# Performance work log

Hardware: AMD Instinct MI355X
Metric: run time of the kernel (lower is better)

## Reference

```python
import jax, jax.numpy as jnp
import numpy as np


def setup_inputs() -> dict:
    key = jax.random.key(0)
    k1, k2 = jax.random.split(key)
    B, S, D = 4, 2048, 1024
    x = jax.random.normal(k1, (B, S, D), dtype=jnp.float32)
    # uniform initializer in keras is small; scale to keep softmax well-behaved
    kernel = jax.random.normal(k2, (3, D, D), dtype=jnp.float32) * 0.02
    return {"x": x, "kernel": kernel}


def reference(x, kernel):
    # x: [B, S, D], kernel: [3, D, D]
    D = x.shape[-1]
    q = jnp.einsum('bsd,de->bse', x, kernel[0])
    k = jnp.einsum('bsd,de->bse', x, kernel[1])
    v = jnp.einsum('bsd,de->bse', x, kernel[2])
    scores = jnp.einsum('bqe,bke->bqk', q, k) / jnp.sqrt(jnp.float32(D))
    attn = jax.nn.softmax(scores, axis=-1)
    return jnp.einsum('bqk,bke->bqe', attn, v)
```

## Files before the change

kernel.cpp:

```cpp
#include <hip/hip_runtime.h>
#include <hip/hip_bf16.h>
#include <cstdint>

typedef __bf16 bf16x8 __attribute__((ext_vector_type(8)));
typedef float f32x4 __attribute__((ext_vector_type(4)));

__device__ __forceinline__ unsigned short f2bf(float f) {
  union { float f; uint32_t u; } a; a.f = f;
  uint32_t r = a.u + 0x7fffu + ((a.u >> 16) & 1u);
  return (unsigned short)(r >> 16);
}
__device__ __forceinline__ void gload_lds16(const unsigned short* g, unsigned short* l) {
  __builtin_amdgcn_global_load_lds(
      (const __attribute__((address_space(1))) void*)g,
      (__attribute__((address_space(3))) void*)l, 16, 0, 0);
}

__global__ void cast_all(const float* __restrict__ x, const float* __restrict__ W,
                         unsigned short* __restrict__ xb, unsigned short* __restrict__ Wt) {
  __shared__ float tile[32][33];
  const int bx = blockIdx.x;
  const int t = threadIdx.x;
  if (bx < 4096) {
    size_t i = ((size_t)bx * 256 + t) * 8;
    float4 a = *(const float4*)(x + i);
    float4 b = *(const float4*)(x + i + 4);
    uint4 o;
    o.x = (uint32_t)f2bf(a.x) | ((uint32_t)f2bf(a.y) << 16);
    o.y = (uint32_t)f2bf(a.z) | ((uint32_t)f2bf(a.w) << 16);
    o.z = (uint32_t)f2bf(b.x) | ((uint32_t)f2bf(b.y) << 16);
    o.w = (uint32_t)f2bf(b.z) | ((uint32_t)f2bf(b.w) << 16);
    *(uint4*)(xb + i) = o;
  } else {
    const int b = bx - 4096;
    const int z = b >> 10;
    const int rest = b & 1023;
    const int bxx = rest & 31, byy = rest >> 5;
    const float* Wz = W + (size_t)z * 1048576;
    unsigned short* Wtz = Wt + (size_t)z * 1048576;
    const int x0 = bxx * 32, y0 = byy * 32;
    const int tx = t & 31, ty = t >> 5;
#pragma unroll
    for (int i = 0; i < 32; i += 8)
      tile[ty + i][tx] = Wz[(size_t)(y0 + ty + i) * 1024 + x0 + tx];
    __syncthreads();
#pragma unroll
    for (int i = 0; i < 32; i += 8)
      Wtz[(size_t)(x0 + ty + i) * 1024 + y0 + tx] = f2bf(tile[tx][ty + i]);
  }
}

template <int MODE>
__global__ void __launch_bounds__(256)
gemm_bt(const unsigned short* __restrict__ Aall,
        const unsigned short* __restrict__ Btall,
        void* __restrict__ Call, unsigned short* __restrict__ VtPtr,
        float* __restrict__ aux,
        int K, int ldc, long sA, long sB, long sC, float scale) {
  __shared__ unsigned short As[2][4096];
  __shared__ unsigned short Bs[2][4096];
  const int t = threadIdx.x;
  const int lane = t & 63;
  const int quad = lane >> 4;
  const int l15 = lane & 15;
  const int wave = t >> 6;
  const int wm = (wave >> 1) * 64;
  const int wn = (wave & 1) * 64;
  const int z = blockIdx.z;

  const unsigned short* A = Aall + (size_t)z * sA + (size_t)blockIdx.x * 128 * K;
  const unsigned short* Bt = Btall + (size_t)z * sB + (size_t)blockIdx.y * 128 * K;

  const int srow = t >> 2;
  const int scol = (((t & 3) ^ ((srow >> 1) & 3)) * 8);
  const unsigned short* ga = A + (size_t)srow * K + scol;
  const unsigned short* gb = Bt + (size_t)srow * K + scol;
  const size_t rowskip = (size_t)64 * K;

  const int aOff = (wm + l15) * 32 + (quad ^ ((l15 >> 1) & 3)) * 8;
  const int bOff = (wn + l15) * 32 + (quad ^ ((l15 >> 1) & 3)) * 8;

  f32x4 acc[4][4];
#pragma unroll
  for (int i = 0; i < 4; i++)
#pragma unroll
    for (int j = 0; j < 4; j++) acc[i][j] = (f32x4){0.f, 0.f, 0.f, 0.f};

  gload_lds16(ga, &As[0][t * 8]);
  gload_lds16(ga + rowskip, &As[0][2048 + t * 8]);
  gload_lds16(gb, &Bs[0][t * 8]);
  gload_lds16(gb + rowskip, &Bs[0][2048 + t * 8]);

  int buf = 0;
  for (int k0 = 0; k0 < K; k0 += 32, buf ^= 1) {
    __syncthreads();
    if (k0 + 32 < K) {
      const int kn = k0 + 32;
      gload_lds16(ga + kn, &As[buf ^ 1][t * 8]);
      gload_lds16(ga + rowskip + kn, &As[buf ^ 1][2048 + t * 8]);
      gload_lds16(gb + kn, &Bs[buf ^ 1][t * 8]);
      gload_lds16(gb + rowskip + kn, &Bs[buf ^ 1][2048 + t * 8]);
    }
    const unsigned short* aB = &As[buf][aOff];
    const unsigned short* bB = &Bs[buf][bOff];
    bf16x8 a[4], b[4];
#pragma unroll
    for (int i = 0; i < 4; i++) a[i] = *(const bf16x8*)(aB + i * 512);
#pragma unroll
    for (int j = 0; j < 4; j++) b[j] = *(const bf16x8*)(bB + j * 512);
#pragma unroll
    for (int i = 0; i < 4; i++)
#pragma unroll
      for (int j = 0; j < 4; j++)
        acc[i][j] = __builtin_amdgcn_mfma_f32_16x16x32_bf16(a[i], b[j], acc[i][j], 0, 0, 0);
  }

  const int mbase = blockIdx.x * 128 + wm + quad * 4;
  const int nbase = blockIdx.y * 128 + wn + l15;

  if (MODE == 4) {
    if (z < 2) {
      unsigned short* C = (unsigned short*)Call + (size_t)z * sC;
#pragma unroll
      for (int mi = 0; mi < 4; mi++)
#pragma unroll
        for (int ni = 0; ni < 4; ni++) {
          const int m = mbase + mi * 16, n = nbase + ni * 16;
#pragma unroll
          for (int r = 0; r < 4; r++)
            C[(size_t)(m + r) * ldc + n] = f2bf(acc[mi][ni][r]);
        }
    } else {
      unsigned short* C = VtPtr;
#pragma unroll
      for (int mi = 0; mi < 4; mi++) {
        const int m = mbase + mi * 16;
        const int b = m >> 11, s = m & 2047;
#pragma unroll
        for (int ni = 0; ni < 4; ni++) {
          const int n = nbase + ni * 16;
          uint2 val;
          val.x = (uint32_t)f2bf(acc[mi][ni][0]) | ((uint32_t)f2bf(acc[mi][ni][1]) << 16);
          val.y = (uint32_t)f2bf(acc[mi][ni][2]) | ((uint32_t)f2bf(acc[mi][ni][3]) << 16);
          *(uint2*)(C + (size_t)b * 2097152 + (size_t)n * 2048 + s) = val;
        }
      }
    }
  } else if (MODE == 5) {
    unsigned short* C = (unsigned short*)Call + (size_t)z * sC;
    const int j = blockIdx.y * 2 + (wn >> 6);
#pragma unroll
    for (int mi = 0; mi < 4; mi++) {
#pragma unroll
      for (int r = 0; r < 4; r++) {
        const int m = mbase + mi * 16 + r;
        float s = 0.f;
#pragma unroll
        for (int ni = 0; ni < 4; ni++) {
          const float e = __expf(acc[mi][ni][r] * scale);
          C[(size_t)m * ldc + nbase + ni * 16] = f2bf(e);
          s += e;
        }
        s += __shfl_xor(s, 1);
        s += __shfl_xor(s, 2);
        s += __shfl_xor(s, 4);
        s += __shfl_xor(s, 8);
        if (l15 == 0) aux[(size_t)j * 8192 + (size_t)z * 2048 + m] = s;
      }
    }
  } else {
    float* C = (float*)Call + (size_t)z * sC;
#pragma unroll
    for (int mi = 0; mi < 4; mi++) {
#pragma unroll
      for (int r = 0; r < 4; r++) {
        const int m = mbase + mi * 16 + r;
        const size_t grow = (size_t)z * 2048 + m;
        float tot = 0.f;
#pragma unroll
        for (int j = 0; j < 32; j++) tot += aux[(size_t)j * 8192 + grow];
        const float inv = 1.f / tot;
#pragma unroll
        for (int ni = 0; ni < 4; ni++)
          C[(size_t)m * ldc + nbase + ni * 16] = acc[mi][ni][r] * inv;
      }
    }
  }
}

extern "C" void kernel_launch(void* const* d_in, const int* in_sizes, int n_in,
                              void* d_out, int out_size, void* d_ws, size_t ws_size,
                              hipStream_t stream) {
  const float* x = (const float*)d_in[0];
  const float* W = (const float*)d_in[1];
  float* out = (float*)d_out;
  char* ws = (char*)d_ws;
  unsigned short* xb = (unsigned short*)(ws);
  unsigned short* Wt = (unsigned short*)(ws + (16ll << 20));
  float* partial     = (float*)(ws + (16ll << 20));
  unsigned short* Q  = (unsigned short*)(ws + (22ll << 20));
  unsigned short* Kb = (unsigned short*)(ws + (38ll << 20));
  unsigned short* Vt = (unsigned short*)(ws + (54ll << 20));
  unsigned short* Sb = (unsigned short*)(ws + (70ll << 20));

  cast_all<<<7168, 256, 0, stream>>>(x, W, xb, Wt);

  gemm_bt<4><<<dim3(64, 8, 3), 256, 0, stream>>>(
      xb, Wt, Q, Vt, nullptr, 1024, 1024, 0L, 1048576L, 8388608L, 1.0f);
  gemm_bt<5><<<dim3(16, 16, 4), 256, 0, stream>>>(
      Q, Kb, Sb, nullptr, partial, 1024, 2048, 2097152L, 2097152L, 4194304L, 0.03125f);
  gemm_bt<6><<<dim3(16, 8, 4), 256, 0, stream>>>(
      Sb, Vt, out, nullptr, partial, 2048, 1024, 4194304L, 2097152L, 2097152L, 1.0f);
}
```

Baseline: 264.0 us.

## Rewrite GEMM as 256x256-tile, 8-wave pipelined kernel with staged prefetch

Replaces the 128x128, 4-wave GEMM with a 256x256-tile, 512-thread kernel. Each wave computes 128x64 and the K step grows to 64, split into two 32-wide halves. Global-to-LDS loads for later tiles are interleaved between MFMA phases, with explicit vmcnt waits, raw s_barrier and setprio around MFMA blocks. The goal is more data reuse per tile and better overlap of memory with compute. The risks are fewer workgroups (as few as 128 for the PV GEMM) on a 256-CU part, plus higher register and LDS pressure.

```diff
diff --git a/kernel.cpp b/kernel.cpp
--- a/kernel.cpp
+++ b/kernel.cpp
@@ -51,94 +51,156 @@
 }
 
 template <int MODE>
-__global__ void __launch_bounds__(256)
-gemm_bt(const unsigned short* __restrict__ Aall,
-        const unsigned short* __restrict__ Btall,
-        void* __restrict__ Call, unsigned short* __restrict__ VtPtr,
-        float* __restrict__ aux,
-        int K, int ldc, long sA, long sB, long sC, float scale) {
-  __shared__ unsigned short As[2][4096];
-  __shared__ unsigned short Bs[2][4096];
+__global__ void __launch_bounds__(512, 2)
+gemm8(const unsigned short* __restrict__ Aall,
+      const unsigned short* __restrict__ Btall,
+      void* __restrict__ Call, unsigned short* __restrict__ VtPtr,
+      float* __restrict__ aux,
+      int K, int ldc, long sA, long sB, long sC, float scale) {
+  __shared__ unsigned short As[2][2][8192];
+  __shared__ unsigned short Bs[2][2][8192];
   const int t = threadIdx.x;
   const int lane = t & 63;
   const int quad = lane >> 4;
   const int l15 = lane & 15;
   const int wave = t >> 6;
-  const int wm = (wave >> 1) * 64;
-  const int wn = (wave & 1) * 64;
+  const int wm = wave >> 2;
+  const int wn = wave & 3;
   const int z = blockIdx.z;
-
-  const unsigned short* A = Aall + (size_t)z * sA + (size_t)blockIdx.x * 128 * K;
-  const unsigned short* Bt = Btall + (size_t)z * sB + (size_t)blockIdx.y * 128 * K;
-
-  const int srow = t >> 2;
-  const int scol = (((t & 3) ^ ((srow >> 1) & 3)) * 8);
-  const unsigned short* ga = A + (size_t)srow * K + scol;
-  const unsigned short* gb = Bt + (size_t)srow * K + scol;
-  const size_t rowskip = (size_t)64 * K;
-
-  const int aOff = (wm + l15) * 32 + (quad ^ ((l15 >> 1) & 3)) * 8;
-  const int bOff = (wn + l15) * 32 + (quad ^ ((l15 >> 1) & 3)) * 8;
-
-  f32x4 acc[4][4];
-#pragma unroll
-  for (int i = 0; i < 4; i++)
-#pragma unroll
-    for (int j = 0; j < 4; j++) acc[i][j] = (f32x4){0.f, 0.f, 0.f, 0.f};
-
-  gload_lds16(ga, &As[0][t * 8]);
-  gload_lds16(ga + rowskip, &As[0][2048 + t * 8]);
-  gload_lds16(gb, &Bs[0][t * 8]);
-  gload_lds16(gb + rowskip, &Bs[0][2048 + t * 8]);
-
-  int buf = 0;
-  for (int k0 = 0; k0 < K; k0 += 32, buf ^= 1) {
-    __syncthreads();
-    if (k0 + 32 < K) {
-      const int kn = k0 + 32;
-      gload_lds16(ga + kn, &As[buf ^ 1][t * 8]);
-      gload_lds16(ga + rowskip + kn, &As[buf ^ 1][2048 + t * 8]);
-      gload_lds16(gb + kn, &Bs[buf ^ 1][t * 8]);
-      gload_lds16(gb + rowskip + kn, &Bs[buf ^ 1][2048 + t * 8]);
-    }
-    const unsigned short* aB = &As[buf][aOff];
-    const unsigned short* bB = &Bs[buf][bOff];
-    bf16x8 a[4], b[4];
-#pragma unroll
-    for (int i = 0; i < 4; i++) a[i] = *(const bf16x8*)(aB + i * 512);
-#pragma unroll
-    for (int j = 0; j < 4; j++) b[j] = *(const bf16x8*)(bB + j * 512);
-#pragma unroll
-    for (int i = 0; i < 4; i++)
-#pragma unroll
-      for (int j = 0; j < 4; j++)
-        acc[i][j] = __builtin_amdgcn_mfma_f32_16x16x32_bf16(a[i], b[j], acc[i][j], 0, 0, 0);
-  }
-
-  const int mbase = blockIdx.x * 128 + wm + quad * 4;
-  const int nbase = blockIdx.y * 128 + wn + l15;
+  const int NT = K >> 6;
+
+  const unsigned short* Ab = Aall + (size_t)z * sA + (size_t)blockIdx.x * 256 * K;
+  const unsigned short* Bb = Btall + (size_t)z * sB + (size_t)blockIdx.y * 256 * K;
+
+  const int sc = (((t & 3) ^ ((t >> 3) & 3)) * 8);
+  const unsigned short* gA = Ab + (size_t)(t >> 2) * K + sc;
+  const unsigned short* gB = Bb + (size_t)(t >> 2) * K + sc;
+  const size_t half2 = (size_t)128 * K;
+
+  const int swz = (quad ^ ((l15 >> 1) & 3)) * 8;
+  const int aRd = (wm * 128 + l15) * 32 + swz;
+  const int bRd = (wn * 64 + l15) * 32 + swz;
+
+  f32x4 acc[8][4];
+#pragma unroll
+  for (int i = 0; i < 8; ++i)
+#pragma unroll
+    for (int j = 0; j < 4; ++j) acc[i][j] = (f32x4){0.f, 0.f, 0.f, 0.f};
+
+#define STG_A(TT, KH) do { \
+    const unsigned short* g_ = gA + (TT) * 64 + (KH) * 32; \
+    unsigned short* d_ = &As[(TT) & 1][KH][t * 8]; \
+    gload_lds16(g_, d_); \
+    gload_lds16(g_ + half2, d_ + 4096); \
+  } while (0)
+#define STG_B(TT, KH) do { \
+    const unsigned short* g_ = gB + (TT) * 64 + (KH) * 32; \
+    unsigned short* d_ = &Bs[(TT) & 1][KH][t * 8]; \
+    gload_lds16(g_, d_); \
+    gload_lds16(g_ + half2, d_ + 4096); \
+  } while (0)
+
+  STG_B(0, 0); STG_A(0, 0); STG_B(0, 1); STG_A(0, 1);
+  if (NT > 1) {
+    STG_B(1, 0); STG_A(1, 0); STG_B(1, 1);
+    asm volatile("s_waitcnt vmcnt(6)" ::: "memory");
+  } else {
+    asm volatile("s_waitcnt vmcnt(0)" ::: "memory");
+  }
+  __builtin_amdgcn_s_barrier();
+
+  for (int kt = 0; kt < NT; ++kt) {
+    const int buf = kt & 1;
+    bf16x8 bb[4], a[4];
+
+#pragma unroll
+    for (int j = 0; j < 4; ++j) bb[j] = *(const bf16x8*)&Bs[buf][0][bRd + j * 512];
+#pragma unroll
+    for (int i = 0; i < 4; ++i) a[i] = *(const bf16x8*)&As[buf][0][aRd + i * 512];
+    if (kt + 1 < NT) STG_A(kt + 1, 1);
+    __builtin_amdgcn_s_barrier();
+    __builtin_amdgcn_s_setprio(1);
+#pragma unroll
+    for (int i = 0; i < 4; ++i)
+#pragma unroll
+      for (int j = 0; j < 4; ++j)
+        acc[i][j] = __builtin_amdgcn_mfma_f32_16x16x32_bf16(a[i], bb[j], acc[i][j], 0, 0, 0);
+    __builtin_amdgcn_s_setprio(0);
+    __builtin_amdgcn_s_barrier();
+
+#pragma unroll
+    for (int i = 0; i < 4; ++i) a[i] = *(const bf16x8*)&As[buf][0][aRd + 2048 + i * 512];
+    if (kt + 2 < NT) STG_B(kt + 2, 0);
+    __builtin_amdgcn_s_barrier();
+    __builtin_amdgcn_s_setprio(1);
+#pragma unroll
+    for (int i = 0; i < 4; ++i)
+#pragma unroll
+      for (int j = 0; j < 4; ++j)
+        acc[4 + i][j] = __builtin_amdgcn_mfma_f32_16x16x32_bf16(a[i], bb[j], acc[4 + i][j], 0, 0, 0);
+    __builtin_amdgcn_s_setprio(0);
+    __builtin_amdgcn_s_barrier();
+
+#pragma unroll
+    for (int j = 0; j < 4; ++j) bb[j] = *(const bf16x8*)&Bs[buf][1][bRd + j * 512];
+#pragma unroll
+    for (int i = 0; i < 4; ++i) a[i] = *(const bf16x8*)&As[buf][1][aRd + i * 512];
+    if (kt + 2 < NT) STG_A(kt + 2, 0);
+    __builtin_amdgcn_s_barrier();
+    __builtin_amdgcn_s_setprio(1);
+#pragma unroll
+    for (int i = 0; i < 4; ++i)
+#pragma unroll
+      for (int j = 0; j < 4; ++j)
+        acc[i][j] = __builtin_amdgcn_mfma_f32_16x16x32_bf16(a[i], bb[j], acc[i][j], 0, 0, 0);
+    __builtin_amdgcn_s_setprio(0);
+    __builtin_amdgcn_s_barrier();
+
+#pragma unroll
+    for (int i = 0; i < 4; ++i) a[i] = *(const bf16x8*)&As[buf][1][aRd + 2048 + i * 512];
+    if (kt + 2 < NT) STG_B(kt + 2, 1);
+    __builtin_amdgcn_s_barrier();
+    __builtin_amdgcn_s_setprio(1);
+#pragma unroll
+    for (int i = 0; i < 4; ++i)
+#pragma unroll
+      for (int j = 0; j < 4; ++j)
+        acc[4 + i][j] = __builtin_amdgcn_mfma_f32_16x16x32_bf16(a[i], bb[j], acc[4 + i][j], 0, 0, 0);
+    __builtin_amdgcn_s_setprio(0);
+    if (kt < NT - 2) {
+      asm volatile("s_waitcnt vmcnt(6)" ::: "memory");
+    } else if (kt == NT - 2) {
+      asm volatile("s_waitcnt vmcnt(0)" ::: "memory");
+    }
+    __builtin_amdgcn_s_barrier();
+  }
+#undef STG_A
+#undef STG_B
+
+  const int mb = blockIdx.x * 256 + wm * 128 + quad * 4;
+  const int nb = blockIdx.y * 256 + wn * 64 + l15;
 
   if (MODE == 4) {
     if (z < 2) {
       unsigned short* C = (unsigned short*)Call + (size_t)z * sC;
 #pragma unroll
-      for (int mi = 0; mi < 4; mi++)
-#pragma unroll
-        for (int ni = 0; ni < 4; ni++) {
-          const int m = mbase + mi * 16, n = nbase + ni * 16;
-#pragma unroll
-          for (int r = 0; r < 4; r++)
+      for (int mi = 0; mi < 8; ++mi)
+#pragma unroll
+        for (int ni = 0; ni < 4; ++ni) {
+          const int m = mb + mi * 16, n = nb + ni * 16;
+#pragma unroll
+          for (int r = 0; r < 4; ++r)
             C[(size_t)(m + r) * ldc + n] = f2bf(acc[mi][ni][r]);
         }
     } else {
       unsigned short* C = VtPtr;
 #pragma unroll
-      for (int mi = 0; mi < 4; mi++) {
-        const int m = mbase + mi * 16;
+      for (int mi = 0; mi < 8; ++mi) {
+        const int m = mb + mi * 16;
         const int b = m >> 11, s = m & 2047;
 #pragma unroll
-        for (int ni = 0; ni < 4; ni++) {
-          const int n = nbase + ni * 16;
+        for (int ni = 0; ni < 4; ++ni) {
+          const int n = nb + ni * 16;
           uint2 val;
           val.x = (uint32_t)f2bf(acc[mi][ni][0]) | ((uint32_t)f2bf(acc[mi][ni][1]) << 16);
           val.y = (uint32_t)f2bf(acc[mi][ni][2]) | ((uint32_t)f2bf(acc[mi][ni][3]) << 16);
@@ -148,17 +210,17 @@
     }
   } else if (MODE == 5) {
     unsigned short* C = (unsigned short*)Call + (size_t)z * sC;
-    const int j = blockIdx.y * 2 + (wn >> 6);
-#pragma unroll
-    for (int mi = 0; mi < 4; mi++) {
-#pragma unroll
-      for (int r = 0; r < 4; r++) {
-        const int m = mbase + mi * 16 + r;
+    const int j = blockIdx.y * 4 + wn;
+#pragma unroll
+    for (int mi = 0; mi < 8; ++mi) {
+#pragma unroll
+      for (int r = 0; r < 4; ++r) {
+        const int m = mb + mi * 16 + r;
         float s = 0.f;
 #pragma unroll
-        for (int ni = 0; ni < 4; ni++) {
+        for (int ni = 0; ni < 4; ++ni) {
           const float e = __expf(acc[mi][ni][r] * scale);
-          C[(size_t)m * ldc + nbase + ni * 16] = f2bf(e);
+          C[(size_t)m * ldc + nb + ni * 16] = f2bf(e);
           s += e;
         }
         s += __shfl_xor(s, 1);
@@ -171,18 +233,18 @@
   } else {
     float* C = (float*)Call + (size_t)z * sC;
 #pragma unroll
-    for (int mi = 0; mi < 4; mi++) {
-#pragma unroll
-      for (int r = 0; r < 4; r++) {
-        const int m = mbase + mi * 16 + r;
+    for (int mi = 0; mi < 8; ++mi) {
+#pragma unroll
+      for (int r = 0; r < 4; ++r) {
+        const int m = mb + mi * 16 + r;
         const size_t grow = (size_t)z * 2048 + m;
         float tot = 0.f;
 #pragma unroll
-        for (int j = 0; j < 32; j++) tot += aux[(size_t)j * 8192 + grow];
+        for (int j = 0; j < 32; ++j) tot += aux[(size_t)j * 8192 + grow];
         const float inv = 1.f / tot;
 #pragma unroll
-        for (int ni = 0; ni < 4; ni++)
-          C[(size_t)m * ldc + nbase + ni * 16] = acc[mi][ni][r] * inv;
+        for (int ni = 0; ni < 4; ++ni)
+          C[(size_t)m * ldc + nb + ni * 16] = acc[mi][ni][r] * inv;
       }
     }
   }
@@ -205,10 +267,10 @@
 
   cast_all<<<7168, 256, 0, stream>>>(x, W, xb, Wt);
 
-  gemm_bt<4><<<dim3(64, 8, 3), 256, 0, stream>>>(
+  gemm8<4><<<dim3(32, 4, 3), 512, 0, stream>>>(
       xb, Wt, Q, Vt, nullptr, 1024, 1024, 0L, 1048576L, 8388608L, 1.0f);
-  gemm_bt<5><<<dim3(16, 16, 4), 256, 0, stream>>>(
+  gemm8<5><<<dim3(8, 8, 4), 512, 0, stream>>>(
       Q, Kb, Sb, nullptr, partial, 1024, 2048, 2097152L, 2097152L, 4194304L, 0.03125f);
-  gemm_bt<6><<<dim3(16, 8, 4), 256, 0, stream>>>(
+  gemm8<6><<<dim3(8, 4, 4), 512, 0, stream>>>(
       Sb, Vt, out, nullptr, partial, 2048, 1024, 4194304L, 2097152L, 2097152L, 1.0f);
 }
```

New measurement: 282.0 us. 6.8% more time.
